# Performance work log

Measured on AMD Instinct MI355X. Metric: run time of the kernel, lower is better.

## Reference

```python
import jax, jax.numpy as jnp
import numpy as np
import math

B, N, D, H, E, EA = 8, 512, 256, 8, 8192, 32
HD = D // H

def focus(d, s, w):
    # gaussian wave focus
    return jnp.exp(-((d - s) ** 2) / (2.0 * w ** 2 + 1e-6))

def setup_inputs() -> dict:
    key = jax.random.key(0)
    ks = jax.random.split(key, 16)
    inp = {
        'x': jax.random.normal(ks[0], (B, N, D), jnp.float32),
        'adj': jax.random.uniform(ks[1], (B, N, N), jnp.float32) * 4.0,
        'edge_index': jax.random.randint(ks[2], (B, 2, E), 0, N),
        'edge_attr': jax.random.normal(ks[3], (B, E, EA), jnp.float32),
        'mask': jnp.ones((B, N), bool),
        'valid_edge_mask': jnp.ones((B, E), bool),
        # parameters
        'qkv_W': jax.random.normal(ks[4], (D, 3 * D), jnp.float32) / math.sqrt(D),
        'qkv_b': jnp.zeros((3 * D,), jnp.float32),
        'ffn1_W': jax.random.normal(ks[5], (EA, EA), jnp.float32) / math.sqrt(EA),
        'ffn1_b': jnp.zeros((EA,), jnp.float32),
        'ffn2_W': jax.random.normal(ks[6], (EA, EA), jnp.float32) / math.sqrt(EA),
        'ffn2_b': jnp.zeros((EA,), jnp.float32),
        'ds_W': jax.random.normal(ks[7], (EA, H), jnp.float32) / math.sqrt(EA),
        'ds_b': jnp.zeros((H,), jnp.float32),
        'dw_W': jax.random.normal(ks[8], (EA, H), jnp.float32) / math.sqrt(EA),
        'dw_b': jnp.zeros((H,), jnp.float32),
        'shifts': jnp.array([0.5 * (i + 1) for i in range(H)], jnp.float32),
        'widths': jnp.ones((H,), jnp.float32),
        'self_loop_W': 1.0 / HD + jax.random.uniform(ks[9], (H,), jnp.float32),
    }
    return inp

def reference(x, adj, edge_index, edge_attr, mask, valid_edge_mask,
              qkv_W, qkv_b, ffn1_W, ffn1_b, ffn2_W, ffn2_b,
              ds_W, ds_b, dw_W, dw_b, shifts, widths, self_loop_W):
    b, n, _ = x.shape
    h, hd = shifts.shape[0], (qkv_W.shape[1] // 3) // shifts.shape[0]
    qkv = (x @ qkv_W + qkv_b).reshape(b, n, 3, h, hd)
    qkv = jnp.transpose(qkv, (2, 0, 3, 1, 4))  # [3,B,H,N,hd]
    Q, K, V = qkv[0], qkv[1], qkv[2]

    # edge FFN applied twice (eval mode: noise/dropout disabled); result feeds
    # edge_mapping in the original but is never used downstream (dead code).

    # edge-modulated shift/width come from raw edge_attr
    delta_shift = jnp.transpose(edge_attr @ ds_W + ds_b, (0, 2, 1))  # [B,H,E]
    delta_width = jnp.transpose(edge_attr @ dw_W + dw_b, (0, 2, 1))  # [B,H,E]

    scores = jnp.einsum('bhnd,bhmd->bhnm', Q, K) / jnp.sqrt(jnp.float32(hd))

    s4 = shifts.reshape(1, h, 1, 1)
    w4 = widths.reshape(1, h, 1, 1)
    baseline_focus = jnp.clip(focus(adj[:, None], s4, w4), 1e-6, None)  # [B,H,N,N]
    adjusted = scores + jnp.log(baseline_focus)

    eu = edge_index[:, 0, :]  # [B,E]
    ev = edge_index[:, 1, :]
    bidx = jnp.arange(b)[:, None]
    edge_dist = adj[bidx, eu, ev]  # [B,E]

    mod_shift = shifts[None, :, None] + delta_shift  # [B,H,E]
    mod_width = widths[None, :, None] + delta_width
    mod_focus = jnp.clip(focus(edge_dist[:, None, :], mod_shift, mod_width), 1e-6, None)
    mod_log = jnp.where(valid_edge_mask[:, None, :], jnp.log(mod_focus), 0.0)  # [B,H,E]

    # scatter: overwrite edge entries with scores + modulated log-focus
    bI = jnp.arange(b)[:, None, None]
    hI = jnp.arange(h)[None, :, None]
    uI = jnp.broadcast_to(eu[:, None, :], (b, h, eu.shape[-1]))
    vI = jnp.broadcast_to(ev[:, None, :], (b, h, ev.shape[-1]))
    adjusted = adjusted.at[bI, hI, uI, vI].set(scores[bI, hI, uI, vI] + mod_log)

    eye = jnp.eye(n, dtype=adjusted.dtype)[None, None]
    adjusted = adjusted + eye * self_loop_W.reshape(1, h, 1, 1)

    mask2d = mask[:, None, :] & mask[:, :, None]  # [B,N,N]
    adjusted = jnp.where(mask2d[:, None], adjusted, -1e6)

    attn = jax.nn.softmax(adjusted, axis=-1)
    out = jnp.einsum('bhnm,bhmd->bhnd', attn, V)
    return jnp.transpose(out, (0, 2, 1, 3)).reshape(b, n, -1)
```

## Files before the change

kernel.cpp:

```cpp
#include <hip/hip_runtime.h>

#define B_ 8
#define N_ 512
#define D_ 256
#define H_ 8
#define HD_ 32
#define E_ 8192
#define EA_ 32

#define LOG1EM6 -13.815510557964274f
#define SCALE 0.17677669529663687f

typedef _Float16 half8 __attribute__((ext_vector_type(8)));
typedef _Float16 half4t __attribute__((ext_vector_type(4)));
typedef __fp16 fp16x2 __attribute__((ext_vector_type(2)));
typedef float f32x16 __attribute__((ext_vector_type(16)));

__global__ __launch_bounds__(256) void prep_kernel(
    int* __restrict__ packT, const float* __restrict__ W,
    _Float16* __restrict__ Wt, const float* __restrict__ adj)
{
    __shared__ float t[64][65];
    const int blk = blockIdx.x;
    const int r  = threadIdx.x >> 4;
    const int c4 = (threadIdx.x & 15) * 4;

    if (blk < 512) {
        const int b = blk >> 6, vt = (blk >> 3) & 7, ut = blk & 7;
        const int u0 = ut * 64, v0 = vt * 64;
        const float* src = adj + ((size_t)b * N_ + u0) * N_ + v0;
#pragma unroll
        for (int it = 0; it < 4; it++) {
            int rr = r + it * 16;
            float4 v = *(const float4*)&src[rr * N_ + c4];
            t[rr][c4 + 0] = v.x; t[rr][c4 + 1] = v.y;
            t[rr][c4 + 2] = v.z; t[rr][c4 + 3] = v.w;
        }
        __syncthreads();
        int* dst = packT + ((size_t)b * N_ + v0) * N_ + u0;
#pragma unroll
        for (int it = 0; it < 4; it++) {
            int rr = r + it * 16;
            int4 pv;
            union { _Float16 f; unsigned short s; } cc;
            cc.f = (_Float16)t[c4 + 0][rr]; pv.x = ((int)cc.s) << 16;
            cc.f = (_Float16)t[c4 + 1][rr]; pv.y = ((int)cc.s) << 16;
            cc.f = (_Float16)t[c4 + 2][rr]; pv.z = ((int)cc.s) << 16;
            cc.f = (_Float16)t[c4 + 3][rr]; pv.w = ((int)cc.s) << 16;
            *(int4*)&dst[rr * N_ + c4] = pv;
        }
    } else {
        const int ti = blk - 512;
        const int k0 = (ti / 12) * 64;
        const int n0 = (ti % 12) * 64;
        const float* src = W + (size_t)k0 * 768 + n0;
#pragma unroll
        for (int it = 0; it < 4; it++) {
            int rr = r + it * 16;
            float4 v = *(const float4*)&src[rr * 768 + c4];
            t[rr][c4 + 0] = v.x; t[rr][c4 + 1] = v.y;
            t[rr][c4 + 2] = v.z; t[rr][c4 + 3] = v.w;
        }
        __syncthreads();
        _Float16* dst = Wt + (size_t)n0 * 256 + k0;
#pragma unroll
        for (int it = 0; it < 4; it++) {
            int rr = r + it * 16;
            half4t hv;
#pragma unroll
            for (int kk = 0; kk < 4; kk++) hv[kk] = (_Float16)t[c4 + kk][rr];
            *(half4t*)&dst[rr * 256 + c4] = hv;
        }
    }
}

__global__ __launch_bounds__(256) void mid_kernel(
    const float* __restrict__ x, const _Float16* __restrict__ Wt,
    const float* __restrict__ bias,
    _Float16* __restrict__ Qf, _Float16* __restrict__ Kf,
    _Float16* __restrict__ Vf,
    const float* __restrict__ edge_attr, const int* __restrict__ edge_index,
    const float* __restrict__ adj,
    const float* __restrict__ ds_W, const float* __restrict__ ds_b,
    const float* __restrict__ dw_W, const float* __restrict__ dw_b,
    const float* __restrict__ shifts, const float* __restrict__ widths,
    float* __restrict__ mlog, int* __restrict__ packT)
{
    extern __shared__ char lds[];
    const int tid = threadIdx.x;
    const int blk = blockIdx.x;

    if (blk < 768) {
        const int m0 = (blk / 12) * 64;
        const int n0 = (blk % 12) * 64;

        const int srow = (tid >> 2) & 63;
        const int kj   = tid & 3;
        const int shb  = (tid >> 1) & 1;
        const int slhi = tid & 1;

#pragma unroll
        for (int it = 0; it < 16; it++) {
            int k4 = kj + 4 * it;
            float4 v = *(const float4*)&x[(size_t)(m0 + srow) * 256 + k4 * 4];
            union { _Float16 h[4]; uint2 u; } c;
            c.h[0] = (_Float16)v.x; c.h[1] = (_Float16)v.y;
            c.h[2] = (_Float16)v.z; c.h[3] = (_Float16)v.w;
            int off = (((srow >> 5) * 16 + it) << 10) +
                      ((slhi * 32 + (srow & 31)) << 4) + shb * 8;
            *(uint2*)(lds + off) = c.u;
        }
#pragma unroll
        for (int it = 0; it < 16; it++) {
            int k4 = kj + 4 * it;
            uint2 v = *(const uint2*)&Wt[(size_t)(n0 + srow) * 256 + k4 * 4];
            int off = 32768 + (((srow >> 5) * 16 + it) << 10) +
                      ((slhi * 32 + (srow & 31)) << 4) + shb * 8;
            *(uint2*)(lds + off) = v;
        }
        __syncthreads();

        const int wv = tid >> 6, lane = tid & 63, hi = lane >> 5;
        const int rb = wv & 1, cb = wv >> 1;
        const int c_base = n0 + cb * 32;
        const int which  = c_base >> 8;
        const int h      = (c_base >> 5) & 7;
        const int b      = m0 >> 9;
        const int ut     = ((m0 & 511) >> 5) + rb;

        f32x16 acc;
#pragma unroll
        for (int r = 0; r < 16; r++) acc[r] = 0.0f;

        if (which < 2) {
#pragma unroll
            for (int ks = 0; ks < 16; ks++) {
                half8 af = *(const half8*)(lds + 32768 + (((cb * 16 + ks) << 10)) + lane * 16);
                half8 bf = *(const half8*)(lds + (((rb * 16 + ks) << 10)) + lane * 16);
                acc = __builtin_amdgcn_mfma_f32_32x32x16_f16(af, bf, acc, 0, 0, 0);
            }
            _Float16* dst = (which == 0) ? Qf : Kf;
            const float sc = (which == 0) ? SCALE : 1.0f;
            size_t pb = (((size_t)(b * H_ + h) * 16 + ut) * 2) * 1024;
#pragma unroll
            for (int kh = 0; kh < 2; kh++) {
                union { _Float16 h[8]; int4 q; } fr;
#pragma unroll
                for (int j = 0; j < 8; j++) {
                    int r = kh * 8 + j;
                    int hd = (r & 3) + 8 * (r >> 2) + 4 * hi;
                    fr.h[j] = (_Float16)((acc[r] + bias[c_base + hd]) * sc);
                }
                *(int4*)((char*)dst + pb + kh * 1024 + lane * 16) = fr.q;
            }
        } else {
#pragma unroll
            for (int ks = 0; ks < 16; ks++) {
                half8 af = *(const half8*)(lds + (((rb * 16 + ks) << 10)) + lane * 16);
                half8 bf = *(const half8*)(lds + 32768 + (((cb * 16 + ks) << 10)) + lane * 16);
                acc = __builtin_amdgcn_mfma_f32_32x32x16_f16(af, bf, acc, 0, 0, 0);
            }
            const float bcol = bias[c_base + (lane & 31)];
            size_t pb = (((size_t)(b * H_ + h) * 16 + ut) * 2) * 1024;
#pragma unroll
            for (int kh = 0; kh < 2; kh++) {
                union { _Float16 h[8]; int4 q; } fr;
#pragma unroll
                for (int j = 0; j < 8; j++)
                    fr.h[j] = (_Float16)(acc[kh * 8 + j] + bcol);
                *(int4*)((char*)Vf + pb + kh * 1024 + lane * 16) = fr.q;
            }
        }
        return;
    }

    float* ea  = (float*)lds;
    float* dsW = ea + 256 * 33;
    float* dwW = dsW + 256;
    const int eb = blk - 768;
    const int b  = eb >> 5;
    const int e0 = (eb & 31) * 256;

    const float* eabase = edge_attr + ((size_t)b * E_ + e0) * EA_;
#pragma unroll
    for (int it = 0; it < 32; it++) {
        int i = tid + it * 256;
        ea[(i >> 5) * 33 + (i & 31)] = eabase[i];
    }
    dsW[tid] = ds_W[tid];
    dwW[tid] = dw_W[tid];
    __syncthreads();

    const int e  = e0 + tid;
    const int eu = edge_index[(size_t)b * 2 * E_ + e];
    const int ev = edge_index[(size_t)b * 2 * E_ + E_ + e];
    const float d = adj[((size_t)b * N_ + eu) * N_ + ev];

    float ds[8], dw[8];
#pragma unroll
    for (int h = 0; h < 8; h++) { ds[h] = ds_b[h]; dw[h] = dw_b[h]; }
#pragma unroll
    for (int k = 0; k < 32; k++) {
        float a = ea[tid * 33 + k];
#pragma unroll
        for (int h = 0; h < 8; h++) {
            ds[h] += a * dsW[k * 8 + h];
            dw[h] += a * dwW[k * 8 + h];
        }
    }
#pragma unroll
    for (int h = 0; h < 8; h++) {
        float ms = shifts[h] + ds[h];
        float mw = widths[h] + dw[h];
        float t  = d - ms;
        float ml = fmaxf(-(t * t) / (2.0f * mw * mw + 1e-6f), LOG1EM6);
        mlog[((size_t)(b * H_ + h)) * E_ + e] = ml;
    }
    union { _Float16 f; unsigned short s; } ab;
    ab.f = (_Float16)d;
    atomicMax(&packT[((size_t)b * N_ + ev) * N_ + eu],
              (((int)ab.s) << 16) | (e + 1));
}

__device__ __forceinline__ unsigned pkf16(float x, float y)
{
    fp16x2 v = __builtin_amdgcn_cvt_pkrtz(x, y);
    union { fp16x2 h; unsigned u; } c; c.h = v; return c.u;
}

__device__ __forceinline__ half8 pack_pfrag(const float* p)
{
    union { unsigned u[4]; half8 h; } r;
    r.u[0] = pkf16(p[0], p[1]);
    r.u[1] = pkf16(p[2], p[3]);
    r.u[2] = pkf16(p[4], p[5]);
    r.u[3] = pkf16(p[6], p[7]);
    return r.h;
}

__device__ __forceinline__ float av_from_pack(int pk)
{
    union { unsigned short s; _Float16 f; } cc;
    cc.s = (unsigned short)(((unsigned)pk) >> 16);
    return (float)cc.f;
}

__global__ __launch_bounds__(512) void attn_kernel(
    const _Float16* __restrict__ Qf, const _Float16* __restrict__ Kf,
    const _Float16* __restrict__ Vf, const int* __restrict__ packT,
    const float* __restrict__ mlog,
    const float* __restrict__ shifts, const float* __restrict__ widths,
    const float* __restrict__ slw_arr, float* __restrict__ out)
{
    __shared__ float ldsO[8][16][64];
    __shared__ float ldsM[8][64];
    __shared__ float ldsS[8][64];

    const int bid  = blockIdx.x;
    const int b    = bid >> 7;
    const int h    = (bid >> 4) & 7;
    const int ut   = bid & 15;
    const int wv   = threadIdx.x >> 6;
    const int lane = threadIdx.x & 63;
    const int hi   = lane >> 5;
    const int u0w  = ut * 32;

    const size_t panel = ((size_t)(b * H_ + h) * 16) * 2048;
    const char* Kp = (const char*)Kf + panel;
    const char* Vp = (const char*)Vf + panel;
    const char* Qp = (const char*)Qf + panel;

    half8 qf0 = *(const half8*)(Qp + (ut * 2 + 0) * 1024 + lane * 16);
    half8 qf1 = *(const half8*)(Qp + (ut * 2 + 1) * 1024 + lane * 16);

    const float s_h   = shifts[h];
    const float w_h   = widths[h];
    const float inv2w = 1.0f / (2.0f * w_h * w_h + 1e-6f);
    const float slw   = slw_arr[h];
    const float* mlg  = mlog + (size_t)(b * H_ + h) * E_;
    const int ucol    = u0w + (lane & 31);
    const int* prow   = packT + (size_t)b * N_ * N_ + ucol;

    f32x16 Oacc;
#pragma unroll
    for (int r = 0; r < 16; r++) Oacc[r] = 0.0f;
    float m = -1e30f, ssum = 0.0f;

#pragma unroll
    for (int i = 0; i < 2; i++) {
        const int vt = wv * 2 + i;
        half8 ka0 = *(const half8*)(Kp + (vt * 2 + 0) * 1024 + lane * 16);
        half8 ka1 = *(const half8*)(Kp + (vt * 2 + 1) * 1024 + lane * 16);
        f32x16 C;
#pragma unroll
        for (int r = 0; r < 16; r++) C[r] = 0.0f;
        C = __builtin_amdgcn_mfma_f32_32x32x16_f16(ka0, qf0, C, 0, 0, 0);
        C = __builtin_amdgcn_mfma_f32_32x32x16_f16(ka1, qf1, C, 0, 0, 0);

        float p[16];
        float pmax = -1e30f;
        const int vbase = vt * 32 + 4 * hi;
#pragma unroll
        for (int r = 0; r < 16; r++) {
            int vg  = vbase + (r & 3) + 8 * (r >> 2);
            int pkr = prow[(size_t)vg * N_];
            int sv  = (pkr & 0xffff) - 1;
            float av = av_from_pack(pkr);
            float ml = mlg[sv < 0 ? 0 : sv];
            float t  = av - s_h;
            float bl = fmaxf(-(t * t) * inv2w, LOG1EM6);
            float sc = C[r] + (sv >= 0 ? ml : bl);
            if (vg == ucol) sc += slw;
            p[r] = sc;
            pmax = fmaxf(pmax, sc);
        }
        pmax = fmaxf(pmax, __shfl_xor(pmax, 32, 64));

        if (!__all(pmax - m <= 8.0f)) {
            float mnew = fmaxf(m, pmax);
            float scl  = __expf(m - mnew);
#pragma unroll
            for (int r = 0; r < 16; r++) {
                int ur = (r & 3) + 8 * (r >> 2) + 4 * hi;
                Oacc[r] *= __shfl(scl, ur, 64);
            }
            ssum *= scl;
            m = mnew;
        }

#pragma unroll
        for (int r = 0; r < 16; r++) {
            p[r] = __expf(p[r] - m);
            ssum += p[r];
        }

        half8 pa0 = pack_pfrag(&p[0]);
        half8 pa1 = pack_pfrag(&p[8]);
        half8 vb0 = *(const half8*)(Vp + (vt * 2 + 0) * 1024 + lane * 16);
        half8 vb1 = *(const half8*)(Vp + (vt * 2 + 1) * 1024 + lane * 16);
        Oacc = __builtin_amdgcn_mfma_f32_32x32x16_f16(pa0, vb0, Oacc, 0, 0, 0);
        Oacc = __builtin_amdgcn_mfma_f32_32x32x16_f16(pa1, vb1, Oacc, 0, 0, 0);
    }

#pragma unroll
    for (int r = 0; r < 16; r++) ldsO[wv][r][lane] = Oacc[r];
    ldsM[wv][lane] = m;
    ldsS[wv][lane] = ssum;
    __syncthreads();

    float ms_[8], ss_[8];
#pragma unroll
    for (int s = 0; s < 8; s++) { ms_[s] = ldsM[s][lane]; ss_[s] = ldsS[s][lane]; }
    float mt = ms_[0];
#pragma unroll
    for (int s = 1; s < 8; s++) mt = fmaxf(mt, ms_[s]);
    float scs[8];
    float denom = 0.0f;
#pragma unroll
    for (int s = 0; s < 8; s++) {
        scs[s] = __expf(ms_[s] - mt);
        denom += ss_[s] * scs[s];
    }
    float stot = denom + __shfl_xor(denom, 32, 64);
    float rs = 1.0f / stot;

#pragma unroll
    for (int rr = 0; rr < 2; rr++) {
        int r  = wv * 2 + rr;
        int ur = (r & 3) + 8 * (r >> 2) + 4 * hi;
        float o = 0.0f;
#pragma unroll
        for (int s = 0; s < 8; s++)
            o += ldsO[s][r][lane] * __shfl(scs[s], ur, 64);
        o *= __shfl(rs, ur, 64);
        int ug = u0w + ur;
        out[((size_t)(b * N_ + ug)) * D_ + h * HD_ + (lane & 31)] = o;
    }
}

extern "C" void kernel_launch(void* const* d_in, const int* in_sizes, int n_in,
                              void* d_out, int out_size, void* d_ws, size_t ws_size,
                              hipStream_t stream)
{
    const float* x          = (const float*)d_in[0];
    const float* adj        = (const float*)d_in[1];
    const int*   edge_index = (const int*)d_in[2];
    const float* edge_attr  = (const float*)d_in[3];
    const float* qkv_W      = (const float*)d_in[6];
    const float* qkv_b      = (const float*)d_in[7];
    const float* ds_W       = (const float*)d_in[12];
    const float* ds_b       = (const float*)d_in[13];
    const float* dw_W       = (const float*)d_in[14];
    const float* dw_b       = (const float*)d_in[15];
    const float* shifts     = (const float*)d_in[16];
    const float* widths     = (const float*)d_in[17];
    const float* slw        = (const float*)d_in[18];
    float* out = (float*)d_out;

    _Float16* Qf   = (_Float16*)d_ws;
    _Float16* Kf   = Qf + (size_t)B_ * H_ * N_ * HD_;
    _Float16* Vf   = Kf + (size_t)B_ * H_ * N_ * HD_;
    float*    mlog = (float*)(Vf + (size_t)B_ * H_ * N_ * HD_);
    int*      packT = (int*)(mlog + (size_t)B_ * H_ * E_);
    _Float16* Wt   = (_Float16*)(packT + (size_t)B_ * N_ * N_);

    prep_kernel<<<dim3(560), 256, 0, stream>>>(packT, qkv_W, Wt, adj);

    hipFuncSetAttribute((const void*)mid_kernel,
                        hipFuncAttributeMaxDynamicSharedMemorySize, 65536);
    mid_kernel<<<dim3(1024), 256, 65536, stream>>>(
        x, Wt, qkv_b, Qf, Kf, Vf,
        edge_attr, edge_index, adj,
        ds_W, ds_b, dw_W, dw_b, shifts, widths, mlog, packT);

    attn_kernel<<<dim3(1024), 512, 0, stream>>>(Qf, Kf, Vf, packT,
                                                mlog, shifts, widths, slw, out);
}
```

Before: 44.84 us.

## Pre-pack x and W into MFMA fragment layout, read directly from global

The prep kernel now converts x to fp16 and writes both x and the QKV weight in the exact MFMA operand fragment layout. The GEMM part of the mid kernel then loads fragments straight from global memory instead of staging through LDS with a barrier. This moves the fp32-to-fp16 conversion earlier and removes the LDS round trip and sync. In exchange it adds an extra global write and read of x, and each fragment is re-read from global or L2 by several blocks.

```diff
diff --git a/kernel.cpp b/kernel.cpp
--- a/kernel.cpp
+++ b/kernel.cpp
@@ -18,14 +18,16 @@
 
 __global__ __launch_bounds__(256) void prep_kernel(
     int* __restrict__ packT, const float* __restrict__ W,
-    _Float16* __restrict__ Wt, const float* __restrict__ adj)
+    _Float16* __restrict__ Wfrag, const float* __restrict__ adj,
+    const float* __restrict__ x, _Float16* __restrict__ xfrag)
 {
     __shared__ float t[64][65];
     const int blk = blockIdx.x;
-    const int r  = threadIdx.x >> 4;
-    const int c4 = (threadIdx.x & 15) * 4;
+    const int tid = threadIdx.x;
 
     if (blk < 512) {
+        const int r  = tid >> 4;
+        const int c4 = (tid & 15) * 4;
         const int b = blk >> 6, vt = (blk >> 3) & 7, ut = blk & 7;
         const int u0 = ut * 64, v0 = vt * 64;
         const float* src = adj + ((size_t)b * N_ + u0) * N_ + v0;
@@ -49,7 +51,9 @@
             cc.f = (_Float16)t[c4 + 3][rr]; pv.w = ((int)cc.s) << 16;
             *(int4*)&dst[rr * N_ + c4] = pv;
         }
-    } else {
+    } else if (blk < 560) {
+        const int r  = tid >> 4;
+        const int c4 = (tid & 15) * 4;
         const int ti = blk - 512;
         const int k0 = (ti / 12) * 64;
         const int n0 = (ti % 12) * 64;
@@ -62,20 +66,43 @@
             t[rr][c4 + 2] = v.z; t[rr][c4 + 3] = v.w;
         }
         __syncthreads();
-        _Float16* dst = Wt + (size_t)n0 * 256 + k0;
+        const int k4  = (k0 >> 2) + (tid & 15);
+        const int ks  = k4 >> 2;
+        const int hb  = (k4 >> 1) & 1;
+        const int lhi = k4 & 1;
 #pragma unroll
         for (int it = 0; it < 4; it++) {
-            int rr = r + it * 16;
-            half4t hv;
-#pragma unroll
-            for (int kk = 0; kk < 4; kk++) hv[kk] = (_Float16)t[c4 + kk][rr];
-            *(half4t*)&dst[rr * 256 + c4] = hv;
+            int rr  = r + it * 16;
+            int col = n0 + rr;
+            union { _Float16 h[4]; uint2 u; } c;
+#pragma unroll
+            for (int kk = 0; kk < 4; kk++) c.h[kk] = (_Float16)t[c4 + kk][rr];
+            int off = (((col >> 5) * 16 + ks) << 10) +
+                      ((lhi * 32 + (col & 31)) << 4) + hb * 8;
+            *(uint2*)((char*)Wfrag + off) = c.u;
+        }
+    } else {
+        const int rt = blk - 560;
+        const float* src = x + (size_t)rt * 32 * 256;
+        char* dstbase = (char*)xfrag + (size_t)rt * 16384;
+#pragma unroll
+        for (int it = 0; it < 8; it++) {
+            int g   = tid + it * 256;
+            int row = g >> 6;
+            int k4  = g & 63;
+            float4 v = *(const float4*)&src[row * 256 + k4 * 4];
+            union { _Float16 h[4]; uint2 u; } c;
+            c.h[0] = (_Float16)v.x; c.h[1] = (_Float16)v.y;
+            c.h[2] = (_Float16)v.z; c.h[3] = (_Float16)v.w;
+            int ks = k4 >> 2, hb = (k4 >> 1) & 1, lhi = k4 & 1;
+            int off = (ks << 10) + ((lhi * 32 + row) << 4) + hb * 8;
+            *(uint2*)(dstbase + off) = c.u;
         }
     }
 }
 
 __global__ __launch_bounds__(256) void mid_kernel(
-    const float* __restrict__ x, const _Float16* __restrict__ Wt,
+    const _Float16* __restrict__ xfrag, const _Float16* __restrict__ Wfrag,
     const float* __restrict__ bias,
     _Float16* __restrict__ Qf, _Float16* __restrict__ Kf,
     _Float16* __restrict__ Vf,
@@ -94,40 +121,19 @@
         const int m0 = (blk / 12) * 64;
         const int n0 = (blk % 12) * 64;
 
-        const int srow = (tid >> 2) & 63;
-        const int kj   = tid & 3;
-        const int shb  = (tid >> 1) & 1;
-        const int slhi = tid & 1;
-
-#pragma unroll
-        for (int it = 0; it < 16; it++) {
-            int k4 = kj + 4 * it;
-            float4 v = *(const float4*)&x[(size_t)(m0 + srow) * 256 + k4 * 4];
-            union { _Float16 h[4]; uint2 u; } c;
-            c.h[0] = (_Float16)v.x; c.h[1] = (_Float16)v.y;
-            c.h[2] = (_Float16)v.z; c.h[3] = (_Float16)v.w;
-            int off = (((srow >> 5) * 16 + it) << 10) +
-                      ((slhi * 32 + (srow & 31)) << 4) + shb * 8;
-            *(uint2*)(lds + off) = c.u;
-        }
-#pragma unroll
-        for (int it = 0; it < 16; it++) {
-            int k4 = kj + 4 * it;
-            uint2 v = *(const uint2*)&Wt[(size_t)(n0 + srow) * 256 + k4 * 4];
-            int off = 32768 + (((srow >> 5) * 16 + it) << 10) +
-                      ((slhi * 32 + (srow & 31)) << 4) + shb * 8;
-            *(uint2*)(lds + off) = v;
-        }
-        __syncthreads();
-
         const int wv = tid >> 6, lane = tid & 63, hi = lane >> 5;
         const int rb = wv & 1, cb = wv >> 1;
+        const int rbg = (m0 >> 5) + rb;
+        const int ctg = (n0 >> 5) + cb;
         const int c_base = n0 + cb * 32;
         const int which  = c_base >> 8;
         const int h      = (c_base >> 5) & 7;
         const int b      = m0 >> 9;
         const int ut     = ((m0 & 511) >> 5) + rb;
 
+        const char* Ap = (const char*)xfrag + ((size_t)rbg << 14);
+        const char* Bp = (const char*)Wfrag + ((size_t)ctg << 14);
+
         f32x16 acc;
 #pragma unroll
         for (int r = 0; r < 16; r++) acc[r] = 0.0f;
@@ -135,8 +141,8 @@
         if (which < 2) {
 #pragma unroll
             for (int ks = 0; ks < 16; ks++) {
-                half8 af = *(const half8*)(lds + 32768 + (((cb * 16 + ks) << 10)) + lane * 16);
-                half8 bf = *(const half8*)(lds + (((rb * 16 + ks) << 10)) + lane * 16);
+                half8 af = *(const half8*)(Bp + (ks << 10) + lane * 16);
+                half8 bf = *(const half8*)(Ap + (ks << 10) + lane * 16);
                 acc = __builtin_amdgcn_mfma_f32_32x32x16_f16(af, bf, acc, 0, 0, 0);
             }
             _Float16* dst = (which == 0) ? Qf : Kf;
@@ -156,8 +162,8 @@
         } else {
 #pragma unroll
             for (int ks = 0; ks < 16; ks++) {
-                half8 af = *(const half8*)(lds + (((rb * 16 + ks) << 10)) + lane * 16);
-                half8 bf = *(const half8*)(lds + 32768 + (((cb * 16 + ks) << 10)) + lane * 16);
+                half8 af = *(const half8*)(Ap + (ks << 10) + lane * 16);
+                half8 bf = *(const half8*)(Bp + (ks << 10) + lane * 16);
                 acc = __builtin_amdgcn_mfma_f32_32x32x16_f16(af, bf, acc, 0, 0, 0);
             }
             const float bcol = bias[c_base + (lane & 31)];
@@ -397,19 +403,21 @@
     const float* slw        = (const float*)d_in[18];
     float* out = (float*)d_out;
 
-    _Float16* Qf   = (_Float16*)d_ws;
-    _Float16* Kf   = Qf + (size_t)B_ * H_ * N_ * HD_;
-    _Float16* Vf   = Kf + (size_t)B_ * H_ * N_ * HD_;
-    float*    mlog = (float*)(Vf + (size_t)B_ * H_ * N_ * HD_);
+    _Float16* Qf    = (_Float16*)d_ws;
+    _Float16* Kf    = Qf + (size_t)B_ * H_ * N_ * HD_;
+    _Float16* Vf    = Kf + (size_t)B_ * H_ * N_ * HD_;
+    float*    mlog  = (float*)(Vf + (size_t)B_ * H_ * N_ * HD_);
     int*      packT = (int*)(mlog + (size_t)B_ * H_ * E_);
-    _Float16* Wt   = (_Float16*)(packT + (size_t)B_ * N_ * N_);
-
-    prep_kernel<<<dim3(560), 256, 0, stream>>>(packT, qkv_W, Wt, adj);
+    _Float16* xfrag = (_Float16*)(packT + (size_t)B_ * N_ * N_);
+    _Float16* Wfrag = xfrag + (size_t)B_ * N_ * D_;
+
+    prep_kernel<<<dim3(688), 256, 0, stream>>>(packT, qkv_W, Wfrag, adj,
+                                               x, xfrag);
 
     hipFuncSetAttribute((const void*)mid_kernel,
                         hipFuncAttributeMaxDynamicSharedMemorySize, 65536);
     mid_kernel<<<dim3(1024), 256, 65536, stream>>>(
-        x, Wt, qkv_b, Qf, Kf, Vf,
+        xfrag, Wfrag, qkv_b, Qf, Kf, Vf,
         edge_attr, edge_index, adj,
         ds_W, ds_b, dw_W, dw_b, shifts, widths, mlog, packT);
 
```

Result: faster. 43.35 us (-3.3%).
